# Optimization experiments

Hardware: AMD Instinct MI355X
Metric: run time of the kernel (lower is better)

## Reference

```python
import jax, jax.numpy as jnp
import numpy as np
from functools import partial

C_IN = 32
KT = 10  # 3*3 taps + bias


def avgpool(x, k):
    B, C, H, W = x.shape
    return x.reshape(B, C, H // k, k, W // k, k).mean(axis=(3, 5))


def conv3x3(x, w, b):
    out = jax.lax.conv_general_dilated(
        x, w, window_strides=(1, 1), padding=[(1, 1), (1, 1)],
        dimension_numbers=("NCHW", "OIHW", "NCHW"))
    return out + b[None, :, None, None]


def conv1x1(x, w, b):
    # w: [O, C, 1, 1]
    return jnp.einsum("bchw,oc->bohw", x, w[:, :, 0, 0]) + b[None, :, None, None]


def predictor(x, w1, b1, w2, b2):
    return x + conv3x3(jax.nn.leaky_relu(conv3x3(x, w1, b1), 0.01), w2, b2)


def flying_conv(x, weight, bias):
    # x: [B,C,H,W]; weight: [B,C,Hb,Wb,9]; bias: [B,C,Hb,Wb]; 8x8 blocks
    B, C, H, W = x.shape
    Hb, Wb = H // 8, W // 8
    xp = jnp.pad(x, ((0, 0), (0, 0), (1, 1), (1, 1)))
    out = jnp.broadcast_to(bias[:, :, :, None, :, None], (B, C, Hb, 8, Wb, 8))
    for k in range(9):
        di, dj = k // 3, k % 3
        xs = xp[:, :, di:di + H, dj:dj + W].reshape(B, C, Hb, 8, Wb, 8)
        out = out + xs * weight[:, :, :, None, :, None, k]
    return out.reshape(B, C, H, W)


def setup_inputs() -> dict:
    key = jax.random.key(0)
    ks = jax.random.split(key, 5)
    B, C, H, W = 4, C_IN, 512, 512
    x = jax.random.normal(ks[0], (B, C, H, W), dtype=jnp.float32)
    pa_w = jax.random.normal(ks[1], (4, 2, C, C, 3, 3), dtype=jnp.float32) * 0.05
    pa_b = jnp.zeros((4, 2, C), dtype=jnp.float32)
    exp_w = jax.random.normal(ks[2], (C * KT, C, 1, 1), dtype=jnp.float32) * 0.05
    exp_b = jnp.zeros((C * KT,), dtype=jnp.float32)
    pw_w = jax.random.normal(ks[3], (C, C, 1, 1), dtype=jnp.float32) * 0.1
    pw_b = jnp.zeros((C,), dtype=jnp.float32)
    return {"x": x, "pa_w": pa_w, "pa_b": pa_b, "exp_w": exp_w,
            "exp_b": exp_b, "pw_w": pw_w, "pw_b": pw_b}


def reference(x, pa_w, pa_b, exp_w, exp_b, pw_w, pw_b):
    B, C, H, W = x.shape
    feat = avgpool(x, 4)  # H/4
    for i in range(4):
        feat = predictor(feat, pa_w[i, 0], pa_b[i, 0], pa_w[i, 1], pa_b[i, 1])
        if i == 1:
            feat = avgpool(feat, 2)  # -> H/8
    wmap = conv1x1(feat, exp_w, exp_b)  # [B, C*10, Hb, Wb]
    Hb, Wb = H // 8, W // 8
    wmap = jnp.tanh(wmap.reshape(B, C, KT, Hb, Wb).transpose(0, 1, 3, 4, 2))
    weight, bias = wmap[..., :9], wmap[..., 9]
    out = flying_conv(x, weight, bias)
    return conv1x1(out, pw_w, pw_b)
```

## Files before the change

kernel.cpp:

```cpp
#include <hip/hip_runtime.h>


#define BATCH 4
#define NCH 32
#define CS128 17680
#define SP128 136
#define CS64 4752
#define SP64 72

__device__ __forceinline__ float fast_tanh(float s) {
  float e = __expf(2.f * s);
  return fmaf(-2.f, __builtin_amdgcn_rcpf(e + 1.f), 1.f);
}

__global__ void zero_kernel(float* __restrict__ p) {
  int i = blockIdx.x * 256 + threadIdx.x;
  *reinterpret_cast<float4*>(p + (size_t)i * 4) = make_float4(0.f, 0.f, 0.f, 0.f);
}

__global__ void prep_kernel(const float* __restrict__ pa_w, const float* __restrict__ exp_w,
                            const float* __restrict__ pw_w, float* __restrict__ wt,
                            float* __restrict__ ewt, float* __restrict__ pwt) {
  int i = blockIdx.x * 256 + threadIdx.x;
  if (i < 73728) {
    int tap = i % 9; int t = i / 9;
    int ci = t & 31; t >>= 5;
    int co = t & 31; int layer = t >> 5;
    wt[((layer * 32 + ci) * 9 + tap) * 32 + co] = pa_w[i];
  } else if (i < 83968) {
    int j = i - 73728; int ci = j & 31; int o = j >> 5;
    ewt[ci * 320 + o] = exp_w[j];
  } else if (i < 84992) {
    int j = i - 83968; int c = j & 31; int o = j >> 5;
    pwt[c * 32 + o] = pw_w[j];
  }
}

__global__ void avgpool4_kernel(const float* __restrict__ x, float* __restrict__ outp) {
  int idx = blockIdx.x * 256 + threadIdx.x;
  if (idx >= BATCH * NCH * 128 * 128) return;
  int ow = idx & 127; int t = idx >> 7; int oh = t & 127; int bc = t >> 7;
  const float* src = x + ((size_t)(bc * 512 + oh * 4)) * 512 + ow * 4;
  float s = 0.f;
#pragma unroll
  for (int r = 0; r < 4; r++) {
    float4 v = *reinterpret_cast<const float4*>(src + (size_t)r * 512);
    s += v.x + v.y + v.z + v.w;
  }
  outp[(size_t)bc * CS128 + (size_t)(oh + 1) * SP128 + ow + 4] = s * 0.0625f;
}

__global__ void avgpool2_kernel(const float* __restrict__ inp, float* __restrict__ outp) {
  int idx = blockIdx.x * 256 + threadIdx.x;
  if (idx >= BATCH * NCH * 64 * 64) return;
  int ow = idx & 63; int t = idx >> 6; int oh = t & 63; int bc = t >> 6;
  const float* sp = inp + (size_t)bc * CS128 + (size_t)(2 * oh + 1) * SP128 + 2 * ow + 4;
  float2 a = *reinterpret_cast<const float2*>(sp);
  float2 b = *reinterpret_cast<const float2*>(sp + SP128);
  outp[(size_t)bc * CS64 + (size_t)(oh + 1) * SP64 + ow + 4] = (a.x + a.y + b.x + b.y) * 0.25f;
}

template <int HS, int SP, int CS, int NCO, bool RELU, bool RES>
__global__ __launch_bounds__(256) void conv3x3v_kernel(
    const float* __restrict__ in, const float* __restrict__ wt,
    const float* __restrict__ bias, const float* __restrict__ res,
    float* __restrict__ out) {
  constexpr int TX = HS / 16;
  constexpr int TY = HS / 32;
  constexpr int GROUPS = 32 / NCO;
  int blk = blockIdx.x;
  int g = blk % GROUPS; int rest = blk / GROUPS;
  int b = rest / (TX * TY); int t = rest % (TX * TY);
  int ty = t / TX, tx = t % TX;
  int og = g * NCO;
  int px = threadIdx.x & 15, py = threadIdx.x >> 4;
  int gy = ty * 32 + py * 2, gx = tx * 16 + px;
  size_t pix = (size_t)(gy + 1) * SP + gx + 4;
  const float* inb = in + (size_t)b * 32 * CS + pix;

  float acc0[NCO], acc1[NCO];
#pragma unroll
  for (int o = 0; o < NCO; o++) { acc0[o] = bias[og + o]; acc1[o] = acc0[o]; }

#pragma unroll 2
  for (int ci = 0; ci < 32; ci++) {
    const float* p = inb + (size_t)ci * CS;
    float v[12];
    v[0] = p[-SP - 1];    v[1] = p[-SP];     v[2] = p[-SP + 1];
    v[3] = p[-1];         v[4] = p[0];       v[5] = p[1];
    v[6] = p[SP - 1];     v[7] = p[SP];      v[8] = p[SP + 1];
    v[9] = p[2 * SP - 1]; v[10] = p[2 * SP]; v[11] = p[2 * SP + 1];
    const float* wr = wt + ci * 288 + og;
#pragma unroll
    for (int tap = 0; tap < 9; tap++) {
      const float* wrow = wr + tap * 32;
#pragma unroll
      for (int o = 0; o < NCO; o++) {
        acc0[o] = fmaf(v[tap], wrow[o], acc0[o]);
        acc1[o] = fmaf(v[tap + 3], wrow[o], acc1[o]);
      }
    }
  }

  float* ob = out + (size_t)b * 32 * CS + (size_t)og * CS + pix;
  const float* rb = RES ? (res + (size_t)b * 32 * CS + (size_t)og * CS + pix) : nullptr;
#pragma unroll
  for (int o = 0; o < NCO; o++) {
    float r0 = acc0[o], r1 = acc1[o];
    if (RELU) { r0 = r0 > 0.f ? r0 : 0.01f * r0; r1 = r1 > 0.f ? r1 : 0.01f * r1; }
    if (RES) { r0 += rb[(size_t)o * CS]; r1 += rb[(size_t)o * CS + SP]; }
    ob[(size_t)o * CS] = r0;
    ob[(size_t)o * CS + SP] = r1;
  }
}

template <int HS, int SP, int CS, int NCO, bool RELU, bool RES>
__global__ __launch_bounds__(256) void conv3x3d_kernel(
    const float* __restrict__ in, const float* __restrict__ wt,
    const float* __restrict__ bias, const float* __restrict__ res,
    float* __restrict__ out) {
  constexpr int TILES = HS / 16;
  constexpr int GROUPS = 32 / NCO;
  int blk = blockIdx.x;
  int g = blk % GROUPS; int rest = blk / GROUPS;
  int b = rest / (TILES * TILES); int t = rest % (TILES * TILES);
  int ty = t / TILES, tx = t % TILES;
  int og = g * NCO;
  int px = threadIdx.x & 15, py = threadIdx.x >> 4;
  int gy = ty * 16 + py, gx = tx * 16 + px;
  size_t pix = (size_t)(gy + 1) * SP + gx + 4;
  const float* inb = in + (size_t)b * 32 * CS + pix;

  float acc[NCO];
#pragma unroll
  for (int o = 0; o < NCO; o++) acc[o] = bias[og + o];

#pragma unroll 2
  for (int ci = 0; ci < 32; ci++) {
    const float* p = inb + (size_t)ci * CS;
    float v[9];
    v[0] = p[-SP - 1]; v[1] = p[-SP]; v[2] = p[-SP + 1];
    v[3] = p[-1];      v[4] = p[0];   v[5] = p[1];
    v[6] = p[SP - 1];  v[7] = p[SP];  v[8] = p[SP + 1];
    const float* wr = wt + ci * 288 + og;
#pragma unroll
    for (int tap = 0; tap < 9; tap++) {
      const float* wrow = wr + tap * 32;
#pragma unroll
      for (int o = 0; o < NCO; o++)
        acc[o] = fmaf(v[tap], wrow[o], acc[o]);
    }
  }

  float* ob = out + (size_t)b * 32 * CS + (size_t)og * CS + pix;
  const float* rb = RES ? (res + (size_t)b * 32 * CS + (size_t)og * CS + pix) : nullptr;
#pragma unroll
  for (int o = 0; o < NCO; o++) {
    float r2 = acc[o];
    if (RELU) r2 = r2 > 0.f ? r2 : 0.01f * r2;
    if (RES) r2 += rb[(size_t)o * CS];
    ob[(size_t)o * CS] = r2;
  }
}

__global__ __launch_bounds__(256) void expander_kernel(
    const float* __restrict__ feat, const float* __restrict__ ewt,
    const float* __restrict__ eb, float* __restrict__ wmap) {
  int idx = blockIdx.x * 256 + threadIdx.x;
  int wq = idx & 15; int t = idx >> 4;
  int o = t % 320; int rest = t / 320;
  int hb = rest & 63; int b = rest >> 6;
  const float* fp = feat + (size_t)b * 32 * CS64 + (size_t)(hb + 1) * SP64 + 4 + wq * 4;
  float s0 = eb[o];
  float s1 = s0, s2 = s0, s3 = s0;
#pragma unroll 8
  for (int ci = 0; ci < 32; ci++) {
    float4 f = *reinterpret_cast<const float4*>(fp + (size_t)ci * CS64);
    float wv = ewt[ci * 320 + o];
    s0 = fmaf(f.x, wv, s0); s1 = fmaf(f.y, wv, s1);
    s2 = fmaf(f.z, wv, s2); s3 = fmaf(f.w, wv, s3);
  }
  float4 r;
  r.x = fast_tanh(s0); r.y = fast_tanh(s1);
  r.z = fast_tanh(s2); r.w = fast_tanh(s3);
  *reinterpret_cast<float4*>(wmap + (size_t)((b * 64 + hb) * 320 + o) * 64 + wq * 4) = r;
}

__global__ __launch_bounds__(256) void fused_fly_pw_kernel(
    const float* __restrict__ x, const float* __restrict__ wmap,
    const float* __restrict__ pwt, const float* __restrict__ pw_b,
    float* __restrict__ out) {
  __shared__ float s_w[8][322];
  int blk = blockIdx.x;
  int wtile = blk & 7; int t = blk >> 3; int hb = t & 63; int b = t >> 6;
  int tid = threadIdx.x;

  const float* wsrc = wmap + (size_t)(b * 64 + hb) * 320 * 64 + wtile * 8;
#pragma unroll
  for (int j = 0; j < 10; j++) {
    int idx = j * 256 + tid;
    int tap = idx >> 3, wb8 = idx & 7;
    s_w[wb8][tap] = wsrc[(size_t)tap * 64 + wb8];
  }
  __syncthreads();

  int p = tid & 31, row = tid >> 5;
  int h = hb * 8 + row;
  int w0 = wtile * 64 + 2 * p;
  int wbl = p >> 2;
  const float* xb = x + (size_t)b * 32 * 262144;
  bool wl_ok = (w0 > 0), wr_ok = (w0 < 510);

  float2 acc[32];
#pragma unroll
  for (int o = 0; o < 32; o++) {
    float bv = pw_b[o];
    acc[o].x = bv; acc[o].y = bv;
  }

  for (int c = 0; c < 32; c++) {
    const float2* w2p = reinterpret_cast<const float2*>(&s_w[wbl][c * 10]);
    float2 w01 = w2p[0], w23 = w2p[1], w45 = w2p[2], w67 = w2p[3], w89 = w2p[4];
    float wv[9];
    wv[0] = w01.x; wv[1] = w01.y; wv[2] = w23.x;
    wv[3] = w23.y; wv[4] = w45.x; wv[5] = w45.y;
    wv[6] = w67.x; wv[7] = w67.y; wv[8] = w89.x;
    float fly0 = w89.y, fly1 = w89.y;

    const float* xc = xb + (size_t)c * 262144;
#pragma unroll
    for (int di = 0; di < 3; di++) {
      int hh = h + di - 1;
      if (hh < 0 || hh >= 512) continue;
      const float* rp = xc + (size_t)hh * 512 + w0;
      float xl = wl_ok ? rp[-1] : 0.f;
      float2 xm = *reinterpret_cast<const float2*>(rp);
      float xr = wr_ok ? rp[2] : 0.f;
      float wa = wv[di * 3 + 0], wb_ = wv[di * 3 + 1], wc = wv[di * 3 + 2];
      fly0 = fmaf(xl,   wa, fly0); fly0 = fmaf(xm.x, wb_, fly0); fly0 = fmaf(xm.y, wc, fly0);
      fly1 = fmaf(xm.x, wa, fly1); fly1 = fmaf(xm.y, wb_, fly1); fly1 = fmaf(xr,   wc, fly1);
    }
    const float* prow = pwt + c * 32;
#pragma unroll
    for (int o = 0; o < 32; o++) {
      float pw = prow[o];
      acc[o].x = fmaf(fly0, pw, acc[o].x);
      acc[o].y = fmaf(fly1, pw, acc[o].y);
    }
  }
  float* ob = out + (size_t)b * 32 * 262144 + (size_t)h * 512 + w0;
#pragma unroll
  for (int o = 0; o < 32; o++)
    *reinterpret_cast<float2*>(ob + (size_t)o * 262144) = acc[o];
}

extern "C" void kernel_launch(void* const* d_in, const int* in_sizes, int n_in,
                              void* d_out, int out_size, void* d_ws, size_t ws_size,
                              hipStream_t stream) {
  const float* x     = (const float*)d_in[0];
  const float* pa_w  = (const float*)d_in[1];
  const float* pa_b  = (const float*)d_in[2];
  const float* exp_w = (const float*)d_in[3];
  const float* exp_b = (const float*)d_in[4];
  const float* pw_w  = (const float*)d_in[5];
  const float* pw_b  = (const float*)d_in[6];
  float* out = (float*)d_out;
  float* ws  = (float*)d_ws;

  float* feat0p = ws;
  float* tmpAp  = feat0p + 2263040;
  float* feat1p = tmpAp + 2263040;
  float* wmap   = feat1p + 608256;
  float* tmpBp  = wmap;
  float* wt     = wmap + 5242880;
  float* ewt    = wt + 73728;
  float* pwt    = ewt + 10240;

  hipLaunchKernelGGL(zero_kernel, dim3(5608), dim3(256), 0, stream, ws);
  hipLaunchKernelGGL(prep_kernel, dim3(332), dim3(256), 0, stream, pa_w, exp_w, pw_w, wt, ewt, pwt);
  hipLaunchKernelGGL(avgpool4_kernel, dim3(8192), dim3(256), 0, stream, x, feat0p);

  for (int i = 0; i < 2; i++) {
    const float* w1 = wt + (size_t)(i * 2 + 0) * 9216;
    const float* b1 = pa_b + (i * 2 + 0) * 32;
    const float* w2 = wt + (size_t)(i * 2 + 1) * 9216;
    const float* b2 = pa_b + (i * 2 + 1) * 32;
    hipLaunchKernelGGL((conv3x3v_kernel<128, SP128, CS128, 4, true, false>),
                       dim3(1024), dim3(256), 0, stream, feat0p, w1, b1, nullptr, tmpAp);
    hipLaunchKernelGGL((conv3x3v_kernel<128, SP128, CS128, 4, false, true>),
                       dim3(1024), dim3(256), 0, stream, tmpAp, w2, b2, feat0p, feat0p);
  }

  hipLaunchKernelGGL(avgpool2_kernel, dim3(2048), dim3(256), 0, stream, feat0p, feat1p);

  for (int i = 2; i < 4; i++) {
    const float* w1 = wt + (size_t)(i * 2 + 0) * 9216;
    const float* b1 = pa_b + (i * 2 + 0) * 32;
    const float* w2 = wt + (size_t)(i * 2 + 1) * 9216;
    const float* b2 = pa_b + (i * 2 + 1) * 32;
    hipLaunchKernelGGL((conv3x3d_kernel<64, SP64, CS64, 2, true, false>),
                       dim3(1024), dim3(256), 0, stream, feat1p, w1, b1, nullptr, tmpBp);
    hipLaunchKernelGGL((conv3x3d_kernel<64, SP64, CS64, 2, false, true>),
                       dim3(1024), dim3(256), 0, stream, tmpBp, w2, b2, feat1p, feat1p);
  }

  hipLaunchKernelGGL(expander_kernel, dim3(5120), dim3(256), 0, stream, feat1p, ewt, exp_b, wmap);

  hipLaunchKernelGGL(fused_fly_pw_kernel, dim3(2048), dim3(256), 0, stream,
                     x, wmap, pwt, pw_b, out);
}
```

Measured before the change: 331.0 us.

## Split fused flying-conv into register-sliding depthwise stage plus LDS-staged pointwise

Restructures the fused flying-conv + pointwise kernel into two phases per pass. First, each thread computes the depthwise 3x3 for one channel and row across 32 columns, sliding float4 loads along the row so each x value is read once instead of overlapping halo reads. The results go to a padded shared array. In the second phase, threads read them back to do the 32-output pointwise accumulation, with each thread owning one column and two rows. This removes redundant global loads of x and the per-pair halo loads, at the cost of extra shared memory (~35KB), two barriers per pass, and scalar rather than float2 output stores.

```diff
diff --git a/kernel.cpp b/kernel.cpp
--- a/kernel.cpp
+++ b/kernel.cpp
@@ -191,6 +191,7 @@
     const float* __restrict__ pwt, const float* __restrict__ pw_b,
     float* __restrict__ out) {
   __shared__ float s_w[8][322];
+  __shared__ float fly_s[8][65][17];
   int blk = blockIdx.x;
   int wtile = blk & 7; int t = blk >> 3; int hb = t & 63; int b = t >> 6;
   int tid = threadIdx.x;
@@ -202,56 +203,113 @@
     int tap = idx >> 3, wb8 = idx & 7;
     s_w[wb8][tap] = wsrc[(size_t)tap * 64 + wb8];
   }
-  __syncthreads();
-
-  int p = tid & 31, row = tid >> 5;
-  int h = hb * 8 + row;
-  int w0 = wtile * 64 + 2 * p;
-  int wbl = p >> 2;
+
+  int h0 = hb * 8;
+  int base = wtile * 64;
   const float* xb = x + (size_t)b * 32 * 262144;
-  bool wl_ok = (w0 > 0), wr_ok = (w0 < 510);
-
-  float2 acc[32];
+
+  int cl = (tid >> 3) & 15;
+  int row = tid & 7;
+  int half = tid >> 7;
+  int cstart = half * 32;
+  int col2 = tid & 63, r4 = tid >> 6;
+
+  float acc0[32], acc1[32];
+#pragma unroll
+  for (int o = 0; o < 32; o++) { acc0[o] = pw_b[o]; acc1[o] = pw_b[o]; }
+
+  for (int pass = 0; pass < 2; pass++) {
+    int c = pass * 16 + cl;
+    const float* xc = xb + (size_t)c * 262144;
+    int hA = h0 + row - 1, hC = h0 + row + 1;
+    bool okA = (hA >= 0);
+    bool okC = (hC < 512);
+    const float* pA = xc + (size_t)hA * 512;
+    const float* pB = xc + (size_t)(h0 + row) * 512;
+    const float* pC = xc + (size_t)hC * 512;
+
+    __syncthreads();
+
+    int c0 = base + cstart;
+    int lc = c0 - 1;
+    float lA = 0.f, lB = 0.f, lC = 0.f;
+    if (lc >= 0) {
+      lA = okA ? pA[lc] : 0.f;
+      lB = pB[lc];
+      lC = okC ? pC[lc] : 0.f;
+    }
+    float4 z4 = make_float4(0.f, 0.f, 0.f, 0.f);
+    float4 cA = okA ? *reinterpret_cast<const float4*>(pA + c0) : z4;
+    float4 cB = *reinterpret_cast<const float4*>(pB + c0);
+    float4 cC = okC ? *reinterpret_cast<const float4*>(pC + c0) : z4;
+
+#pragma unroll
+    for (int k2 = 0; k2 < 4; k2++) {
+      int wb8 = (cstart >> 3) + k2;
+      const float* wp = &s_w[wb8][c * 10];
+      float wv0 = wp[0], wv1 = wp[1], wv2 = wp[2], wv3 = wp[3], wv4 = wp[4];
+      float wv5 = wp[5], wv6 = wp[6], wv7 = wp[7], wv8 = wp[8], wv9 = wp[9];
+#pragma unroll
+      for (int kk = 0; kk < 2; kk++) {
+        int k = k2 * 2 + kk;
+        float4 nA, nB, nC;
+        if (k < 7) {
+          int nc = c0 + 4 * (k + 1);
+          nA = okA ? *reinterpret_cast<const float4*>(pA + nc) : z4;
+          nB = *reinterpret_cast<const float4*>(pB + nc);
+          nC = okC ? *reinterpret_cast<const float4*>(pC + nc) : z4;
+        } else {
+          int rc = c0 + 32;
+          bool okR = (rc < 512);
+          nA = z4; nB = z4; nC = z4;
+          nA.x = (okA && okR) ? pA[rc] : 0.f;
+          nB.x = okR ? pB[rc] : 0.f;
+          nC.x = (okC && okR) ? pC[rc] : 0.f;
+        }
+        float f0 = wv9, f1 = wv9, f2 = wv9, f3 = wv9;
+        f0 = fmaf(lA, wv0, f0);   f0 = fmaf(cA.x, wv1, f0); f0 = fmaf(cA.y, wv2, f0);
+        f0 = fmaf(lB, wv3, f0);   f0 = fmaf(cB.x, wv4, f0); f0 = fmaf(cB.y, wv5, f0);
+        f0 = fmaf(lC, wv6, f0);   f0 = fmaf(cC.x, wv7, f0); f0 = fmaf(cC.y, wv8, f0);
+        f1 = fmaf(cA.x, wv0, f1); f1 = fmaf(cA.y, wv1, f1); f1 = fmaf(cA.z, wv2, f1);
+        f1 = fmaf(cB.x, wv3, f1); f1 = fmaf(cB.y, wv4, f1); f1 = fmaf(cB.z, wv5, f1);
+        f1 = fmaf(cC.x, wv6, f1); f1 = fmaf(cC.y, wv7, f1); f1 = fmaf(cC.z, wv8, f1);
+        f2 = fmaf(cA.y, wv0, f2); f2 = fmaf(cA.z, wv1, f2); f2 = fmaf(cA.w, wv2, f2);
+        f2 = fmaf(cB.y, wv3, f2); f2 = fmaf(cB.z, wv4, f2); f2 = fmaf(cB.w, wv5, f2);
+        f2 = fmaf(cC.y, wv6, f2); f2 = fmaf(cC.z, wv7, f2); f2 = fmaf(cC.w, wv8, f2);
+        f3 = fmaf(cA.z, wv0, f3); f3 = fmaf(cA.w, wv1, f3); f3 = fmaf(nA.x, wv2, f3);
+        f3 = fmaf(cB.z, wv3, f3); f3 = fmaf(cB.w, wv4, f3); f3 = fmaf(nB.x, wv5, f3);
+        f3 = fmaf(cC.z, wv6, f3); f3 = fmaf(cC.w, wv7, f3); f3 = fmaf(nC.x, wv8, f3);
+        int colw = cstart + 4 * k;
+        fly_s[row][colw + 0][cl] = f0;
+        fly_s[row][colw + 1][cl] = f1;
+        fly_s[row][colw + 2][cl] = f2;
+        fly_s[row][colw + 3][cl] = f3;
+        lA = cA.w; lB = cB.w; lC = cC.w;
+        cA = nA; cB = nB; cC = nC;
+      }
+    }
+    __syncthreads();
+
+#pragma unroll
+    for (int cc = 0; cc < 16; cc++) {
+      float fa = fly_s[r4][col2][cc];
+      float fb = fly_s[r4 + 4][col2][cc];
+      const float* prow = pwt + (pass * 16 + cc) * 32;
+#pragma unroll
+      for (int o = 0; o < 32; o++) {
+        float pw = prow[o];
+        acc0[o] = fmaf(fa, pw, acc0[o]);
+        acc1[o] = fmaf(fb, pw, acc1[o]);
+      }
+    }
+  }
+
+  float* ob = out + (size_t)b * 32 * 262144 + (size_t)(h0 + r4) * 512 + base + col2;
 #pragma unroll
   for (int o = 0; o < 32; o++) {
-    float bv = pw_b[o];
-    acc[o].x = bv; acc[o].y = bv;
-  }
-
-  for (int c = 0; c < 32; c++) {
-    const float2* w2p = reinterpret_cast<const float2*>(&s_w[wbl][c * 10]);
-    float2 w01 = w2p[0], w23 = w2p[1], w45 = w2p[2], w67 = w2p[3], w89 = w2p[4];
-    float wv[9];
-    wv[0] = w01.x; wv[1] = w01.y; wv[2] = w23.x;
-    wv[3] = w23.y; wv[4] = w45.x; wv[5] = w45.y;
-    wv[6] = w67.x; wv[7] = w67.y; wv[8] = w89.x;
-    float fly0 = w89.y, fly1 = w89.y;
-
-    const float* xc = xb + (size_t)c * 262144;
-#pragma unroll
-    for (int di = 0; di < 3; di++) {
-      int hh = h + di - 1;
-      if (hh < 0 || hh >= 512) continue;
-      const float* rp = xc + (size_t)hh * 512 + w0;
-      float xl = wl_ok ? rp[-1] : 0.f;
-      float2 xm = *reinterpret_cast<const float2*>(rp);
-      float xr = wr_ok ? rp[2] : 0.f;
-      float wa = wv[di * 3 + 0], wb_ = wv[di * 3 + 1], wc = wv[di * 3 + 2];
-      fly0 = fmaf(xl,   wa, fly0); fly0 = fmaf(xm.x, wb_, fly0); fly0 = fmaf(xm.y, wc, fly0);
-      fly1 = fmaf(xm.x, wa, fly1); fly1 = fmaf(xm.y, wb_, fly1); fly1 = fmaf(xr,   wc, fly1);
-    }
-    const float* prow = pwt + c * 32;
-#pragma unroll
-    for (int o = 0; o < 32; o++) {
-      float pw = prow[o];
-      acc[o].x = fmaf(fly0, pw, acc[o].x);
-      acc[o].y = fmaf(fly1, pw, acc[o].y);
-    }
-  }
-  float* ob = out + (size_t)b * 32 * 262144 + (size_t)h * 512 + w0;
-#pragma unroll
-  for (int o = 0; o < 32; o++)
-    *reinterpret_cast<float2*>(ob + (size_t)o * 262144) = acc[o];
+    ob[(size_t)o * 262144] = acc0[o];
+    ob[(size_t)o * 262144 + 2048] = acc1[o];
+  }
 }
 
 extern "C" void kernel_launch(void* const* d_in, const int* in_sizes, int n_in,
```

Result: slower. 474.0 us (+43.2%).

## Split fused flying-conv and pointwise conv into two kernels

Applied to the files above, without the earlier changes.

Splits the fused flying-conv plus 1x1 pointwise kernel in two. The first kernel computes the per-block 3x3 conv with four outputs per thread using float4 loads and writes the intermediate into the output buffer. The second kernel reads it back and applies the 32x32 pointwise mix in place. This removes the 64-register accumulator pressure and the per-channel pointwise FMAs from the stencil kernel, at the cost of an extra full write and read of a 128MB intermediate through global memory.

```diff
diff --git a/kernel.cpp b/kernel.cpp
--- a/kernel.cpp
+++ b/kernel.cpp
@@ -186,9 +186,8 @@
   *reinterpret_cast<float4*>(wmap + (size_t)((b * 64 + hb) * 320 + o) * 64 + wq * 4) = r;
 }
 
-__global__ __launch_bounds__(256) void fused_fly_pw_kernel(
+__global__ __launch_bounds__(128) void fly_kernel(
     const float* __restrict__ x, const float* __restrict__ wmap,
-    const float* __restrict__ pwt, const float* __restrict__ pw_b,
     float* __restrict__ out) {
   __shared__ float s_w[8][322];
   int blk = blockIdx.x;
@@ -197,61 +196,81 @@
 
   const float* wsrc = wmap + (size_t)(b * 64 + hb) * 320 * 64 + wtile * 8;
 #pragma unroll
-  for (int j = 0; j < 10; j++) {
-    int idx = j * 256 + tid;
+  for (int j = 0; j < 20; j++) {
+    int idx = j * 128 + tid;
     int tap = idx >> 3, wb8 = idx & 7;
     s_w[wb8][tap] = wsrc[(size_t)tap * 64 + wb8];
   }
   __syncthreads();
 
-  int p = tid & 31, row = tid >> 5;
+  int p = tid & 15, row = tid >> 4;
   int h = hb * 8 + row;
-  int w0 = wtile * 64 + 2 * p;
-  int wbl = p >> 2;
+  int w0 = wtile * 64 + 4 * p;
+  int wbl = p >> 1;
   const float* xb = x + (size_t)b * 32 * 262144;
-  bool wl_ok = (w0 > 0), wr_ok = (w0 < 510);
-
-  float2 acc[32];
-#pragma unroll
-  for (int o = 0; o < 32; o++) {
-    float bv = pw_b[o];
-    acc[o].x = bv; acc[o].y = bv;
-  }
-
+  float* ob = out + (size_t)b * 32 * 262144 + (size_t)h * 512 + w0;
+  bool wl_ok = (w0 > 0), wr_ok = (w0 < 508);
+  int hm = h - 1, hp = h + 1;
+  bool okA = (hm >= 0), okC = (hp < 512);
+  float4 z4 = make_float4(0.f, 0.f, 0.f, 0.f);
+
+#pragma unroll 2
   for (int c = 0; c < 32; c++) {
-    const float2* w2p = reinterpret_cast<const float2*>(&s_w[wbl][c * 10]);
-    float2 w01 = w2p[0], w23 = w2p[1], w45 = w2p[2], w67 = w2p[3], w89 = w2p[4];
-    float wv[9];
-    wv[0] = w01.x; wv[1] = w01.y; wv[2] = w23.x;
-    wv[3] = w23.y; wv[4] = w45.x; wv[5] = w45.y;
-    wv[6] = w67.x; wv[7] = w67.y; wv[8] = w89.x;
-    float fly0 = w89.y, fly1 = w89.y;
+    const float* wp = &s_w[wbl][c * 10];
+    float wv0 = wp[0], wv1 = wp[1], wv2 = wp[2], wv3 = wp[3], wv4 = wp[4];
+    float wv5 = wp[5], wv6 = wp[6], wv7 = wp[7], wv8 = wp[8], wv9 = wp[9];
 
     const float* xc = xb + (size_t)c * 262144;
-#pragma unroll
-    for (int di = 0; di < 3; di++) {
-      int hh = h + di - 1;
-      if (hh < 0 || hh >= 512) continue;
-      const float* rp = xc + (size_t)hh * 512 + w0;
-      float xl = wl_ok ? rp[-1] : 0.f;
-      float2 xm = *reinterpret_cast<const float2*>(rp);
-      float xr = wr_ok ? rp[2] : 0.f;
-      float wa = wv[di * 3 + 0], wb_ = wv[di * 3 + 1], wc = wv[di * 3 + 2];
-      fly0 = fmaf(xl,   wa, fly0); fly0 = fmaf(xm.x, wb_, fly0); fly0 = fmaf(xm.y, wc, fly0);
-      fly1 = fmaf(xm.x, wa, fly1); fly1 = fmaf(xm.y, wb_, fly1); fly1 = fmaf(xr,   wc, fly1);
-    }
-    const float* prow = pwt + c * 32;
-#pragma unroll
-    for (int o = 0; o < 32; o++) {
-      float pw = prow[o];
-      acc[o].x = fmaf(fly0, pw, acc[o].x);
-      acc[o].y = fmaf(fly1, pw, acc[o].y);
-    }
-  }
-  float* ob = out + (size_t)b * 32 * 262144 + (size_t)h * 512 + w0;
-#pragma unroll
-  for (int o = 0; o < 32; o++)
-    *reinterpret_cast<float2*>(ob + (size_t)o * 262144) = acc[o];
+    const float* pA = xc + (size_t)hm * 512 + w0;
+    const float* pB = xc + (size_t)h * 512 + w0;
+    const float* pC = xc + (size_t)hp * 512 + w0;
+    float4 mA = okA ? *reinterpret_cast<const float4*>(pA) : z4;
+    float4 mB = *reinterpret_cast<const float4*>(pB);
+    float4 mC = okC ? *reinterpret_cast<const float4*>(pC) : z4;
+    float lA = (okA && wl_ok) ? pA[-1] : 0.f;
+    float lB = wl_ok ? pB[-1] : 0.f;
+    float lC = (okC && wl_ok) ? pC[-1] : 0.f;
+    float rA = (okA && wr_ok) ? pA[4] : 0.f;
+    float rB = wr_ok ? pB[4] : 0.f;
+    float rC = (okC && wr_ok) ? pC[4] : 0.f;
+
+    float f0 = wv9, f1 = wv9, f2 = wv9, f3 = wv9;
+    f0 = fmaf(lA,   wv0, f0); f0 = fmaf(mA.x, wv1, f0); f0 = fmaf(mA.y, wv2, f0);
+    f0 = fmaf(lB,   wv3, f0); f0 = fmaf(mB.x, wv4, f0); f0 = fmaf(mB.y, wv5, f0);
+    f0 = fmaf(lC,   wv6, f0); f0 = fmaf(mC.x, wv7, f0); f0 = fmaf(mC.y, wv8, f0);
+    f1 = fmaf(mA.x, wv0, f1); f1 = fmaf(mA.y, wv1, f1); f1 = fmaf(mA.z, wv2, f1);
+    f1 = fmaf(mB.x, wv3, f1); f1 = fmaf(mB.y, wv4, f1); f1 = fmaf(mB.z, wv5, f1);
+    f1 = fmaf(mC.x, wv6, f1); f1 = fmaf(mC.y, wv7, f1); f1 = fmaf(mC.z, wv8, f1);
+    f2 = fmaf(mA.y, wv0, f2); f2 = fmaf(mA.z, wv1, f2); f2 = fmaf(mA.w, wv2, f2);
+    f2 = fmaf(mB.y, wv3, f2); f2 = fmaf(mB.z, wv4, f2); f2 = fmaf(mB.w, wv5, f2);
+    f2 = fmaf(mC.y, wv6, f2); f2 = fmaf(mC.z, wv7, f2); f2 = fmaf(mC.w, wv8, f2);
+    f3 = fmaf(mA.z, wv0, f3); f3 = fmaf(mA.w, wv1, f3); f3 = fmaf(rA,   wv2, f3);
+    f3 = fmaf(mB.z, wv3, f3); f3 = fmaf(mB.w, wv4, f3); f3 = fmaf(rB,   wv5, f3);
+    f3 = fmaf(mC.z, wv6, f3); f3 = fmaf(mC.w, wv7, f3); f3 = fmaf(rC,   wv8, f3);
+
+    *reinterpret_cast<float4*>(ob + (size_t)c * 262144) = make_float4(f0, f1, f2, f3);
+  }
+}
+
+__global__ __launch_bounds__(256) void pw_inplace_kernel(
+    const float* __restrict__ pwt, const float* __restrict__ pw_b,
+    float* __restrict__ out) {
+  int idx = blockIdx.x * 256 + threadIdx.x;
+  size_t base = (size_t)(idx >> 18) * 32 * 262144 + (idx & 262143);
+  float f[32];
+#pragma unroll
+  for (int c = 0; c < 32; c++) f[c] = out[base + (size_t)c * 262144];
+  float acc[32];
+#pragma unroll
+  for (int o = 0; o < 32; o++) acc[o] = pw_b[o];
+  for (int c = 0; c < 32; c++) {
+    const float* wrow = pwt + c * 32;
+#pragma unroll
+    for (int o = 0; o < 32; o++)
+      acc[o] = fmaf(f[c], wrow[o], acc[o]);
+  }
+#pragma unroll
+  for (int o = 0; o < 32; o++) out[base + (size_t)o * 262144] = acc[o];
 }
 
 extern "C" void kernel_launch(void* const* d_in, const int* in_sizes, int n_in,
@@ -306,6 +325,6 @@
 
   hipLaunchKernelGGL(expander_kernel, dim3(5120), dim3(256), 0, stream, feat1p, ewt, exp_b, wmap);
 
-  hipLaunchKernelGGL(fused_fly_pw_kernel, dim3(2048), dim3(256), 0, stream,
-                     x, wmap, pwt, pw_b, out);
-}
+  hipLaunchKernelGGL(fly_kernel, dim3(2048), dim3(128), 0, stream, x, wmap, out);
+  hipLaunchKernelGGL(pw_inplace_kernel, dim3(4096), dim3(256), 0, stream, pwt, pw_b, out);
+}
```

Result: slower. 399.4 us (+20.7%).
